# Performance work log

Measured on AMD Instinct MI355X. Metric: run time of the kernel, lower is better.

## Reference

```python
import jax, jax.numpy as jnp
import numpy as np

IN_CH, OUT_CH, K, STRIDE = 128, 256, 3, 1

def setup_inputs() -> dict:
    key = jax.random.key(0)
    kx, kw = jax.random.split(key)
    x = jax.random.normal(kx, (32, IN_CH, 56, 56), dtype=jnp.float32)
    # xavier_uniform: bound = sqrt(6 / (fan_in + fan_out)), fans include receptive field
    fan_in = IN_CH * K * K
    fan_out = OUT_CH * K * K
    bound = float(np.sqrt(6.0 / (fan_in + fan_out)))
    weight = jax.random.uniform(kw, (OUT_CH, IN_CH, K, K), dtype=jnp.float32,
                                minval=-bound, maxval=bound)
    bias = jnp.zeros((OUT_CH,), dtype=jnp.float32)
    return {"x": x, "weight": weight, "bias": bias}

def reference(x, weight, bias):
    # VALID (no-padding) conv, stride STRIDE, NCHW layout, OIHW kernel
    out = jax.lax.conv_general_dilated(
        x, weight,
        window_strides=(STRIDE, STRIDE),
        padding="VALID",
        dimension_numbers=("NCHW", "OIHW", "NCHW"))
    return out + bias[None, :, None, None]
```

## Files before the change

kernel.cpp:

```cpp
#include <hip/hip_runtime.h>
#include <hip/hip_bf16.h>
#include <stdint.h>

#define NB    32
#define CIN   128
#define HIN   56
#define HW    (HIN*HIN)
#define OCH   256
#define OHW   54
#define SPB   (OHW*OHW)
#define KSZ   (CIN*9)
#define BM    256
#define BN    256
#define BK    64
#define NKS   (KSZ/BK)
#define TOTC  (NB*SPB)
#define NT    365

typedef __attribute__((ext_vector_type(8))) short bf16x8;
typedef __attribute__((ext_vector_type(4))) float f32x4;

typedef __attribute__((address_space(1))) const uint32_t g_u32;
typedef __attribute__((address_space(3))) uint32_t l_u32;
static __device__ __forceinline__ void gl_lds16(const void* g, void* l) {
    __builtin_amdgcn_global_load_lds((g_u32*)g, (l_u32*)l, 16, 0, 0);
}

__global__ void xpose_cast(const float* __restrict__ x, __hip_bfloat16* __restrict__ xt) {
    __shared__ float tile[32][33];
    const int hw0 = blockIdx.x * 32;
    const int c0  = blockIdx.y * 32;
    const int n   = blockIdx.z;
    const int tx = threadIdx.x, ty = threadIdx.y;
    const float* xp = x + ((size_t)n*CIN + c0)*HW + hw0;
    #pragma unroll
    for (int i = ty; i < 32; i += 8)
        tile[i][tx] = xp[(size_t)i*HW + tx];
    __syncthreads();
    const int t = ty*32 + tx;
    const int hwl = t >> 3, q = t & 7;
    ushort4 v;
    v.x = __bfloat16_as_ushort(__float2bfloat16(tile[q*4+0][hwl]));
    v.y = __bfloat16_as_ushort(__float2bfloat16(tile[q*4+1][hwl]));
    v.z = __bfloat16_as_ushort(__float2bfloat16(tile[q*4+2][hwl]));
    v.w = __bfloat16_as_ushort(__float2bfloat16(tile[q*4+3][hwl]));
    __hip_bfloat16* op = xt + ((size_t)n*HW + hw0 + hwl)*CIN + c0 + q*4;
    *(ushort4*)op = v;
}

__global__ void wcast(const float* __restrict__ w, __hip_bfloat16* __restrict__ wt) {
    int tid = blockIdx.x*256 + threadIdx.x;
    if (tid >= OCH*KSZ) return;
    int oc = tid / KSZ, r = tid % KSZ;
    int pos = r >> 7, ic = r & 127;
    wt[tid] = __float2bfloat16(w[((size_t)(oc*CIN + ic))*9 + pos]);
}

__global__ __launch_bounds__(512, 2)
void conv_mfma(const __hip_bfloat16* __restrict__ xt,
               const __hip_bfloat16* __restrict__ wt,
               const float* __restrict__ bias,
               float* __restrict__ out) {
    __shared__ uint4 smem[8192];

    const int t = threadIdx.x;
    const int tile = blockIdx.x;
    const int lane = t & 63, wid = t >> 6;
    const int wm = wid >> 2, wn = wid & 3;
    const int lr = lane & 15, lq = lane >> 4;

    const __hip_bfloat16* asrc[4];
    const __hip_bfloat16* bsrc[4];
    #pragma unroll
    for (int i = 0; i < 4; ++i) {
        int p = i*512 + t;
        int row = p >> 3, g = (p & 7) ^ (row & 7);
        asrc[i] = wt + (size_t)row*KSZ + g*8;
        int colg = tile*BN + row; if (colg >= TOTC) colg = TOTC - 1;
        int n = colg / SPB, rem = colg - n*SPB;
        int oh = rem / OHW, ow = rem - oh*OHW;
        bsrc[i] = xt + ((size_t)(n*HIN + oh)*HIN + ow)*CIN + g*8;
    }

    auto issueTile = [&](int ks) {
        uint4* Ab = smem + (ks & 1)*4096;
        uint4* Bb = Ab + 2048;
        const int pos = ks >> 1;
        const int kh = pos / 3, kw = pos - kh*3;
        const int aoff = ks*BK;
        const int boff = (kh*HIN + kw)*CIN + (ks & 1)*64;
        #pragma unroll
        for (int i = 0; i < 4; ++i) gl_lds16(asrc[i] + aoff, Ab + i*512 + t);
        #pragma unroll
        for (int i = 0; i < 4; ++i) gl_lds16(bsrc[i] + boff, Bb + i*512 + t);
    };

    f32x4 acc[8][4];
    #pragma unroll
    for (int i = 0; i < 8; ++i)
        #pragma unroll
        for (int j = 0; j < 4; ++j)
            acc[i][j] = (f32x4){0.f, 0.f, 0.f, 0.f};

    issueTile(0);
    asm volatile("s_waitcnt vmcnt(0)" ::: "memory");
    __builtin_amdgcn_s_barrier();

    #define MFMA_BF16 __builtin_amdgcn_mfma_f32_16x16x32_bf16
    #define RD_A(dst, MIB, KK) \
        { int ra = wm*128 + (MIB)*16 + lr; \
          dst = *(bf16x8*)&Ab[ra*8 + (((KK)*4 + lq) ^ (ra & 7))]; }
    #define RD_B(dst, NI, KK) \
        { int rb = wn*64 + (NI)*16 + lr; \
          dst = *(bf16x8*)&Bb[rb*8 + (((KK)*4 + lq) ^ (rb & 7))]; }
    #define PH_SYNC() \
        __builtin_amdgcn_s_barrier(); \
        asm volatile("s_waitcnt lgkmcnt(0)"); \
        __builtin_amdgcn_sched_barrier(0);
    #define MFMA16(AARR, MIB, BARR) \
        __builtin_amdgcn_s_setprio(1); \
        _Pragma("unroll") \
        for (int ii = 0; ii < 4; ++ii) \
            _Pragma("unroll") \
            for (int ni = 0; ni < 4; ++ni) \
                acc[(MIB)+ii][ni] = MFMA_BF16(AARR[ii], BARR[ni], acc[(MIB)+ii][ni], 0, 0, 0); \
        __builtin_amdgcn_s_setprio(0); \
        __builtin_amdgcn_s_barrier();

    for (int ks = 0; ks < NKS; ++ks) {
        const uint4* Ab = smem + (ks & 1)*4096;
        const uint4* Bb = Ab + 2048;
        bf16x8 a[4], b[4];

        RD_A(a[0], 0, 0) RD_A(a[1], 1, 0) RD_A(a[2], 2, 0) RD_A(a[3], 3, 0)
        RD_B(b[0], 0, 0) RD_B(b[1], 1, 0) RD_B(b[2], 2, 0) RD_B(b[3], 3, 0)
        if (ks + 1 < NKS) issueTile(ks + 1);
        PH_SYNC()
        MFMA16(a, 0, b)

        RD_A(a[0], 4, 0) RD_A(a[1], 5, 0) RD_A(a[2], 6, 0) RD_A(a[3], 7, 0)
        PH_SYNC()
        MFMA16(a, 4, b)

        RD_A(a[0], 0, 1) RD_A(a[1], 1, 1) RD_A(a[2], 2, 1) RD_A(a[3], 3, 1)
        RD_B(b[0], 0, 1) RD_B(b[1], 1, 1) RD_B(b[2], 2, 1) RD_B(b[3], 3, 1)
        PH_SYNC()
        MFMA16(a, 0, b)

        RD_A(a[0], 4, 1) RD_A(a[1], 5, 1) RD_A(a[2], 6, 1) RD_A(a[3], 7, 1)
        PH_SYNC()
        __builtin_amdgcn_s_setprio(1);
        #pragma unroll
        for (int ii = 0; ii < 4; ++ii)
            #pragma unroll
            for (int ni = 0; ni < 4; ++ni)
                acc[4+ii][ni] = MFMA_BF16(a[ii], b[ni], acc[4+ii][ni], 0, 0, 0);
        __builtin_amdgcn_s_setprio(0);
        if (ks + 1 < NKS)
            asm volatile("s_waitcnt vmcnt(0)" ::: "memory");
        __builtin_amdgcn_s_barrier();
    }

    float (*eps)[260] = (float (*)[260])smem;
    const int cl4 = (t & 63) * 4;
    const int rsub = t >> 6;
    const int colg = tile*BN + cl4;
    int nn = 0, sp = 0;
    if (colg < TOTC) { nn = colg / SPB; sp = colg - nn*SPB; }
    #pragma unroll
    for (int h = 0; h < 4; ++h) {
        if (wm == (h >> 1)) {
            const int mib = (h & 1) * 4;
            #pragma unroll
            for (int ii = 0; ii < 4; ++ii) {
                int rl = ii*16 + lq*4;
                #pragma unroll
                for (int ni = 0; ni < 4; ++ni) {
                    int cl = wn*64 + ni*16 + lr;
                    #pragma unroll
                    for (int r = 0; r < 4; ++r)
                        eps[rl + r][cl] = acc[mib + ii][ni][r];
                }
            }
        }
        __syncthreads();
        if (colg < TOTC) {
            #pragma unroll
            for (int pass = 0; pass < 8; ++pass) {
                int rl = pass*8 + rsub;
                int rg = h*64 + rl;
                f32x4 v = *(f32x4*)&eps[rl][cl4];
                v = v + bias[rg];
                *(f32x4*)&out[((size_t)nn*OCH + rg)*SPB + sp] = v;
            }
        }
        __syncthreads();
    }
}

__global__ void conv_naive(const float* __restrict__ x, const float* __restrict__ w,
                           const float* __restrict__ bias, float* __restrict__ out) {
    size_t tid = (size_t)blockIdx.x*256 + threadIdx.x;
    const size_t total = (size_t)NB*OCH*SPB;
    if (tid >= total) return;
    int col = (int)(tid % SPB);
    int oc  = (int)((tid / SPB) % OCH);
    int n   = (int)(tid / ((size_t)SPB*OCH));
    int oh = col / OHW, ow = col % OHW;
    float s = bias[oc];
    for (int ic = 0; ic < CIN; ++ic)
        #pragma unroll
        for (int kh = 0; kh < 3; ++kh)
            #pragma unroll
            for (int kw = 0; kw < 3; ++kw)
                s += x[((size_t)(n*CIN+ic)*HIN + oh+kh)*HIN + ow+kw]
                   * w[((size_t)(oc*CIN+ic)*3 + kh)*3 + kw];
    out[tid] = s;
}

extern "C" void kernel_launch(void* const* d_in, const int* in_sizes, int n_in,
                              void* d_out, int out_size, void* d_ws, size_t ws_size,
                              hipStream_t stream) {
    const float* x    = (const float*)d_in[0];
    const float* w    = (const float*)d_in[1];
    const float* bias = (const float*)d_in[2];
    float* out = (float*)d_out;

    const size_t xt_bytes = (size_t)NB*HW*CIN*sizeof(__hip_bfloat16);
    const size_t wt_bytes = (size_t)OCH*KSZ*sizeof(__hip_bfloat16);

    if (ws_size >= xt_bytes + wt_bytes) {
        __hip_bfloat16* xt  = (__hip_bfloat16*)d_ws;
        __hip_bfloat16* wtp = (__hip_bfloat16*)((char*)d_ws + xt_bytes);
        hipLaunchKernelGGL(xpose_cast, dim3(HW/32, CIN/32, NB), dim3(32, 8), 0, stream, x, xt);
        hipLaunchKernelGGL(wcast, dim3((OCH*KSZ + 255)/256), dim3(256), 0, stream, w, wtp);
        hipLaunchKernelGGL(conv_mfma, dim3(NT), dim3(512), 0, stream, xt, wtp, bias, out);
    } else {
        size_t total = (size_t)NB*OCH*SPB;
        hipLaunchKernelGGL(conv_naive, dim3((unsigned)((total + 255)/256)), dim3(256), 0, stream,
                           x, w, bias, out);
    }
}
```

Before: 101.3 us.

## Split tile loads into K-halves and interleave global-to-LDS prefetch with MFMA phases

Reorganizes the shared-memory layout so each 64-wide K tile is stored as two 32-wide halves with a 4-way XOR swizzle. The next tile's global-to-LDS loads are spread across the four MFMA phases of each iteration, and partial vmcnt waits let the second half compute while the later halves are still arriving. This replaces the full vmcnt(0) drain at the end of each iteration and is meant to overlap memory latency with compute more finely. The cost is more complex wait counting, and a wrong vmcnt value could read LDS data that has not finished loading.

```diff
diff --git a/kernel.cpp b/kernel.cpp
--- a/kernel.cpp
+++ b/kernel.cpp
@@ -69,30 +69,33 @@
     const int wm = wid >> 2, wn = wid & 3;
     const int lr = lane & 15, lq = lane >> 4;
 
-    const __hip_bfloat16* asrc[4];
-    const __hip_bfloat16* bsrc[4];
-    #pragma unroll
-    for (int i = 0; i < 4; ++i) {
-        int p = i*512 + t;
-        int row = p >> 3, g = (p & 7) ^ (row & 7);
-        asrc[i] = wt + (size_t)row*KSZ + g*8;
+    const __hip_bfloat16* aptr[2];
+    const __hip_bfloat16* bptr[2];
+    #pragma unroll
+    for (int i = 0; i < 2; ++i) {
+        int q = i*512 + t;
+        int row = q >> 2, j = q & 3;
+        int ls = j ^ (row & 3);
+        aptr[i] = wt + (size_t)row*KSZ + ls*8;
         int colg = tile*BN + row; if (colg >= TOTC) colg = TOTC - 1;
         int n = colg / SPB, rem = colg - n*SPB;
         int oh = rem / OHW, ow = rem - oh*OHW;
-        bsrc[i] = xt + ((size_t)(n*HIN + oh)*HIN + ow)*CIN + g*8;
-    }
-
-    auto issueTile = [&](int ks) {
-        uint4* Ab = smem + (ks & 1)*4096;
-        uint4* Bb = Ab + 2048;
-        const int pos = ks >> 1;
-        const int kh = pos / 3, kw = pos - kh*3;
-        const int aoff = ks*BK;
-        const int boff = (kh*HIN + kw)*CIN + (ks & 1)*64;
-        #pragma unroll
-        for (int i = 0; i < 4; ++i) gl_lds16(asrc[i] + aoff, Ab + i*512 + t);
-        #pragma unroll
-        for (int i = 0; i < 4; ++i) gl_lds16(bsrc[i] + boff, Bb + i*512 + t);
+        bptr[i] = xt + ((size_t)(n*HIN + oh)*HIN + ow)*CIN + ls*8;
+    }
+
+    auto issueU = [&](int ks, int mat, int X) {
+        uint4* dst = smem + (ks & 1)*4096 + mat*2048 + X*1024 + t;
+        if (mat == 0) {
+            const int off = ks*BK + X*32;
+            gl_lds16(aptr[0] + off, dst);
+            gl_lds16(aptr[1] + off, dst + 512);
+        } else {
+            const int pos = ks >> 1;
+            const int kh = pos / 3, kw = pos - kh*3;
+            const int off = (kh*HIN + kw)*CIN + (ks & 1)*64 + X*32;
+            gl_lds16(bptr[0] + off, dst);
+            gl_lds16(bptr[1] + off, dst + 512);
+        }
     };
 
     f32x4 acc[8][4];
@@ -102,63 +105,71 @@
         for (int j = 0; j < 4; ++j)
             acc[i][j] = (f32x4){0.f, 0.f, 0.f, 0.f};
 
-    issueTile(0);
-    asm volatile("s_waitcnt vmcnt(0)" ::: "memory");
-    __builtin_amdgcn_s_barrier();
-
     #define MFMA_BF16 __builtin_amdgcn_mfma_f32_16x16x32_bf16
-    #define RD_A(dst, MIB, KK) \
-        { int ra = wm*128 + (MIB)*16 + lr; \
-          dst = *(bf16x8*)&Ab[ra*8 + (((KK)*4 + lq) ^ (ra & 7))]; }
-    #define RD_B(dst, NI, KK) \
-        { int rb = wn*64 + (NI)*16 + lr; \
-          dst = *(bf16x8*)&Bb[rb*8 + (((KK)*4 + lq) ^ (rb & 7))]; }
-    #define PH_SYNC() \
+    #define RD_A4(arr, MIB, KK) \
+        _Pragma("unroll") \
+        for (int ii = 0; ii < 4; ++ii) { \
+            int ra = wm*128 + ((MIB)+ii)*16 + lr; \
+            arr[ii] = *(bf16x8*)&Ab[(KK)*1024 + ra*4 + (lq ^ (ra & 3))]; \
+        }
+    #define RD_B4(arr, KK) \
+        _Pragma("unroll") \
+        for (int ni = 0; ni < 4; ++ni) { \
+            int rb = wn*64 + ni*16 + lr; \
+            arr[ni] = *(bf16x8*)&Bb[(KK)*1024 + rb*4 + (lq ^ (rb & 3))]; \
+        }
+    #define PH_OPEN() \
         __builtin_amdgcn_s_barrier(); \
         asm volatile("s_waitcnt lgkmcnt(0)"); \
         __builtin_amdgcn_sched_barrier(0);
-    #define MFMA16(AARR, MIB, BARR) \
+    #define MFMA_BLK(AARR, MIB, BARR) \
         __builtin_amdgcn_s_setprio(1); \
         _Pragma("unroll") \
         for (int ii = 0; ii < 4; ++ii) \
             _Pragma("unroll") \
             for (int ni = 0; ni < 4; ++ni) \
                 acc[(MIB)+ii][ni] = MFMA_BF16(AARR[ii], BARR[ni], acc[(MIB)+ii][ni], 0, 0, 0); \
-        __builtin_amdgcn_s_setprio(0); \
-        __builtin_amdgcn_s_barrier();
+        __builtin_amdgcn_s_setprio(0);
+
+    issueU(0, 0, 0); issueU(0, 1, 0); issueU(0, 0, 1); issueU(0, 1, 1);
+    asm volatile("s_waitcnt vmcnt(4)" ::: "memory");
+    __builtin_amdgcn_s_barrier();
+    __builtin_amdgcn_sched_barrier(0);
 
     for (int ks = 0; ks < NKS; ++ks) {
         const uint4* Ab = smem + (ks & 1)*4096;
         const uint4* Bb = Ab + 2048;
+        const bool pf = (ks + 1 < NKS);
         bf16x8 a[4], b[4];
 
-        RD_A(a[0], 0, 0) RD_A(a[1], 1, 0) RD_A(a[2], 2, 0) RD_A(a[3], 3, 0)
-        RD_B(b[0], 0, 0) RD_B(b[1], 1, 0) RD_B(b[2], 2, 0) RD_B(b[3], 3, 0)
-        if (ks + 1 < NKS) issueTile(ks + 1);
-        PH_SYNC()
-        MFMA16(a, 0, b)
-
-        RD_A(a[0], 4, 0) RD_A(a[1], 5, 0) RD_A(a[2], 6, 0) RD_A(a[3], 7, 0)
-        PH_SYNC()
-        MFMA16(a, 4, b)
-
-        RD_A(a[0], 0, 1) RD_A(a[1], 1, 1) RD_A(a[2], 2, 1) RD_A(a[3], 3, 1)
-        RD_B(b[0], 0, 1) RD_B(b[1], 1, 1) RD_B(b[2], 2, 1) RD_B(b[3], 3, 1)
-        PH_SYNC()
-        MFMA16(a, 0, b)
-
-        RD_A(a[0], 4, 1) RD_A(a[1], 5, 1) RD_A(a[2], 6, 1) RD_A(a[3], 7, 1)
-        PH_SYNC()
-        __builtin_amdgcn_s_setprio(1);
-        #pragma unroll
-        for (int ii = 0; ii < 4; ++ii)
-            #pragma unroll
-            for (int ni = 0; ni < 4; ++ni)
-                acc[4+ii][ni] = MFMA_BF16(a[ii], b[ni], acc[4+ii][ni], 0, 0, 0);
-        __builtin_amdgcn_s_setprio(0);
-        if (ks + 1 < NKS)
-            asm volatile("s_waitcnt vmcnt(0)" ::: "memory");
-        __builtin_amdgcn_s_barrier();
+        RD_A4(a, 0, 0) RD_B4(b, 0)
+        if (pf) issueU(ks + 1, 0, 0);
+        PH_OPEN()
+        MFMA_BLK(a, 0, b)
+        __builtin_amdgcn_s_barrier();
+
+        RD_A4(a, 4, 0)
+        if (pf) issueU(ks + 1, 1, 0);
+        PH_OPEN()
+        MFMA_BLK(a, 4, b)
+        if (pf) asm volatile("s_waitcnt vmcnt(4)" ::: "memory");
+        else    asm volatile("s_waitcnt vmcnt(0)" ::: "memory");
+        __builtin_amdgcn_s_barrier();
+        __builtin_amdgcn_sched_barrier(0);
+
+        RD_A4(a, 0, 1) RD_B4(b, 1)
+        if (pf) issueU(ks + 1, 0, 1);
+        PH_OPEN()
+        MFMA_BLK(a, 0, b)
+        __builtin_amdgcn_s_barrier();
+
+        RD_A4(a, 4, 1)
+        if (pf) issueU(ks + 1, 1, 1);
+        PH_OPEN()
+        MFMA_BLK(a, 4, b)
+        if (pf) asm volatile("s_waitcnt vmcnt(4)" ::: "memory");
+        __builtin_amdgcn_s_barrier();
+        __builtin_amdgcn_sched_barrier(0);
     }
 
     float (*eps)[260] = (float (*)[260])smem;
```

Measured after the change: 101.1 us. No clear change (-0.2%).
